# Kernel tuning notes

Measured on AMD Instinct MI355X. Metric: run time of the kernel, lower is better.

## Reference

```python
import jax, jax.numpy as jnp
import numpy as np

EPS = 1e-5
DN = ('NCHW', 'OIHW', 'NCHW')


def conv3x3(x, w, b):
    y = jax.lax.conv_general_dilated(x, w, window_strides=(1, 1), padding='SAME',
                                     dimension_numbers=DN)
    return y + b[None, :, None, None]


def bn_relu(x, g, be, m, v):
    # inference-mode BatchNorm2d followed by ReLU, folded into one FMA
    inv = g / jnp.sqrt(v + EPS)
    return jax.nn.relu(x * inv[None, :, None, None] + (be - m * inv)[None, :, None, None])


def haar_idwt2(cA, cH, cV, cD):
    # pywt.idwt2(coeffs, 'db1'): cH = detail along rows (axis -2), cV = detail along cols (axis -1)
    # Exact Haar synthesis -> 2x2 pixel blocks (pixel-shuffle style, no CPU round-trip)
    p00 = (cA + cH + cV + cD) * 0.5  # (2i,   2j)
    p01 = (cA + cH - cV - cD) * 0.5  # (2i,   2j+1)
    p10 = (cA - cH + cV - cD) * 0.5  # (2i+1, 2j)
    p11 = (cA - cH - cV + cD) * 0.5  # (2i+1, 2j+1)
    B, C, H, W = cA.shape
    even = jnp.stack([p00, p01], axis=-1).reshape(B, C, H, 2 * W)
    odd = jnp.stack([p10, p11], axis=-1).reshape(B, C, H, 2 * W)
    return jnp.stack([even, odd], axis=-2).reshape(B, C, 2 * H, 2 * W)


def setup_inputs() -> dict:
    key = jax.random.key(0)
    ks = jax.random.split(key, 24)
    B, IN_C, OUT_C, H, W = 16, 128, 64, 64, 64
    d = {}
    d['x'] = jax.random.normal(ks[0], (B, IN_C, H, W), jnp.float32)
    d['s'] = jax.random.normal(ks[1], (B, OUT_C, 2 * H, 2 * W), jnp.float32)
    # input_convdwt: Conv(in_c -> 4*in_c) + BN
    d['w1'] = jax.random.normal(ks[2], (4 * IN_C, IN_C, 3, 3), jnp.float32) * 0.05
    d['b1'] = jax.random.normal(ks[3], (4 * IN_C,), jnp.float32) * 0.05
    d['g1'] = jax.random.uniform(ks[4], (4 * IN_C,), jnp.float32, 0.5, 1.5)
    d['be1'] = jax.random.normal(ks[5], (4 * IN_C,), jnp.float32) * 0.05
    d['m1'] = jax.random.normal(ks[6], (4 * IN_C,), jnp.float32) * 0.05
    d['v1'] = jax.random.uniform(ks[7], (4 * IN_C,), jnp.float32, 0.5, 1.5)
    # s_con: Conv(in_c -> out_c) + BN
    d['ws'] = jax.random.normal(ks[8], (OUT_C, IN_C, 3, 3), jnp.float32) * 0.05
    d['bs'] = jax.random.normal(ks[9], (OUT_C,), jnp.float32) * 0.05
    d['gs'] = jax.random.uniform(ks[10], (OUT_C,), jnp.float32, 0.5, 1.5)
    d['bes'] = jax.random.normal(ks[11], (OUT_C,), jnp.float32) * 0.05
    d['ms'] = jax.random.normal(ks[12], (OUT_C,), jnp.float32) * 0.05
    d['vs'] = jax.random.uniform(ks[13], (OUT_C,), jnp.float32, 0.5, 1.5)
    # conv: Conv(in_c -> out_c) + BN (applied to concat(s, s_out))
    d['w2'] = jax.random.normal(ks[14], (OUT_C, IN_C, 3, 3), jnp.float32) * 0.05
    d['b2'] = jax.random.normal(ks[15], (OUT_C,), jnp.float32) * 0.05
    d['g2'] = jax.random.uniform(ks[16], (OUT_C,), jnp.float32, 0.5, 1.5)
    d['be2'] = jax.random.normal(ks[17], (OUT_C,), jnp.float32) * 0.05
    d['m2'] = jax.random.normal(ks[18], (OUT_C,), jnp.float32) * 0.05
    d['v2'] = jax.random.uniform(ks[19], (OUT_C,), jnp.float32, 0.5, 1.5)
    return d


def reference(x, s, w1, b1, g1, be1, m1, v1,
              ws, bs, gs, bes, ms, vs,
              w2, b2, g2, be2, m2, v2):
    # input_convdwt: conv -> BN -> ReLU, channels in_c -> 4*in_c
    h = bn_relu(conv3x3(x, w1, b1), g1, be1, m1, v1)
    c = h.shape[1]
    q = c // 4
    cA, cH, cV, cD = h[:, :q], h[:, q:2 * q], h[:, 2 * q:3 * q], h[:, 3 * q:]
    idwt_out = haar_idwt2(cA, cH, cV, cD)  # (B, in_c, 2H, 2W)
    # skip-connection branch (s is not None)
    s_out = bn_relu(conv3x3(idwt_out, ws, bs), gs, bes, ms, vs)  # (B, out_c, 2H, 2W)
    concat = jnp.concatenate([s, s_out], axis=1)                  # (B, in_c, 2H, 2W)
    decoder_output = bn_relu(conv3x3(concat, w2, b2), g2, be2, m2, v2)
    return decoder_output
```

## Files before the change

kernel.cpp:

```cpp
#include <hip/hip_runtime.h>
#include <hip/hip_bf16.h>

typedef __attribute__((ext_vector_type(8))) short short8;
typedef __attribute__((ext_vector_type(4))) float f32x4;
typedef unsigned short u16;

#define EPSV 1e-5f

__device__ __forceinline__ u16 f2bf(float f) {
    __hip_bfloat16 h = __float2bfloat16(f);
    return *reinterpret_cast<u16*>(&h);
}

#define GLOAD_LDS16(g, l)                                                      \
    __builtin_amdgcn_global_load_lds(                                          \
        (const __attribute__((address_space(1))) void*)(g),                    \
        (__attribute__((address_space(3))) void*)(l), 16, 0, 0)

__global__ void cvt_kernel(const float* __restrict__ src, u16* __restrict__ dst,
                           int C, int H, int W, int units) {
    int u = blockIdx.x * 256 + threadIdx.x;
    if (u >= units) return;
    int kb = u & 3;
    int p  = u >> 2;
    int x  = p % W;  p /= W;
    int y  = p % H;  p /= H;
    int n  = p & 15;
    int cc = p >> 4;
    short8 v;
#pragma unroll
    for (int j = 0; j < 8; ++j)
        v[j] = (short)f2bf(src[(((size_t)n * C + cc * 32 + kb * 8 + j) * H + y) * W + x]);
    *(short8*)(dst + ((((size_t)cc * 16 + n) * H + y) * W + x) * 32 + kb * 8) = v;
}

__global__ void repack_w1_kernel(const float* __restrict__ w1, u16* __restrict__ wf) {
    int u = blockIdx.x * 256 + threadIdx.x;
    if (u >= 4 * 8 * 9 * 4 * 64) return;
    int l = u & 63;
    int r = u >> 6;
    int ciC = r & 3;  r >>= 2;
    int t   = r % 9;  r /= 9;
    int bt  = r & 7;
    int cc  = r >> 3;
    int co  = (bt >> 1) * 128 + cc * 32 + (bt & 1) * 16 + (l & 15);
    int ci0 = ciC * 32 + (l >> 4) * 8;
    short8 v;
#pragma unroll
    for (int e = 0; e < 8; ++e)
        v[e] = (short)f2bf(w1[((size_t)co * 128 + ci0 + e) * 9 + t]);
    *(short8*)(wf + (size_t)u * 8) = v;
}

__global__ void repack_wg_kernel(const float* __restrict__ w, u16* __restrict__ wf) {
    int u = blockIdx.x * 256 + threadIdx.x;
    if (u >= 4 * 9 * 4 * 64) return;
    int l = u & 63;
    int r = u >> 6;
    int ciC = r & 3;  r >>= 2;
    int t   = r % 9;
    int bt  = r / 9;
    int co  = bt * 16 + (l & 15);
    int ci0 = ciC * 32 + (l >> 4) * 8;
    short8 v;
#pragma unroll
    for (int e = 0; e < 8; ++e)
        v[e] = (short)f2bf(w[((size_t)co * 128 + ci0 + e) * 9 + t]);
    *(short8*)(wf + (size_t)u * 8) = v;
}

__global__ __launch_bounds__(256, 2)
void conv1_mfma_kernel(const u16* __restrict__ inb, const u16* __restrict__ wf,
                       const float* __restrict__ bb, const float* __restrict__ gg,
                       const float* __restrict__ bee, const float* __restrict__ mm,
                       const float* __restrict__ vv, u16* __restrict__ ob) {
    const int tile = blockIdx.x;
    const int cc   = blockIdx.y;
    const int n    = blockIdx.z;
    const int x0   = (tile & 3) * 16;
    const int y0   = (tile >> 2) * 8;
    const int tid  = threadIdx.x;
    const int lane = tid & 63;
    const int wid  = tid >> 6;
    const int wm   = wid >> 1;
    const int wc   = wid & 1;
    const int kb   = lane >> 4;
    const int xl   = lane & 15;

    __shared__ float4 lds4[720];
    __shared__ float4 wlds[2][1536];
    const short8* ldsr  = (const short8*)lds4;
    const short8* wldsr = (const short8*)wlds;

    f32x4 acc[4][4];
#pragma unroll
    for (int j = 0; j < 4; ++j)
#pragma unroll
        for (int q = 0; q < 4; ++q) acc[j][q] = (f32x4){0.f, 0.f, 0.f, 0.f};

    float4 sreg[3];
    auto load_stage = [&](int ciC) {
#pragma unroll
        for (int p = 0; p < 3; ++p) {
            int e = p * 256 + tid;
            float4 v = make_float4(0.f, 0.f, 0.f, 0.f);
            if (e < 720) {
                int pix = e >> 2, ke = e & 3;
                int yy = pix / 18;
                int xx = pix - yy * 18;
                int gy = y0 - 1 + yy, gx = x0 - 1 + xx;
                if ((unsigned)gy < 64u && (unsigned)gx < 64u)
                    v = *(const float4*)(inb + ((((size_t)ciC * 16 + n) * 64 + gy) * 64 + gx) * 32 + ke * 8);
            }
            sreg[p] = v;
        }
    };
    auto write_stage = [&]() {
#pragma unroll
        for (int p = 0; p < 3; ++p) {
            int e = p * 256 + tid;
            if (e < 720) lds4[e ^ ((e >> 2) & 7)] = sreg[p];
        }
    };
    auto stage_w = [&](int ciC, int dx, int buf) {
#pragma unroll
        for (int i = 0; i < 6; ++i) {
            int seg = wid * 6 + i;
            int bt  = seg / 3;
            int dy  = seg - bt * 3;
            int t   = dy * 3 + dx;
            const u16* gp = wf + (size_t)((cc * 8 + bt) * 9 + t) * 2048 + ciC * 512 + lane * 8;
            GLOAD_LDS16(gp, &wlds[buf][seg * 64]);
        }
    };

    load_stage(0);
    stage_w(0, 0, 0);
    for (int ciC = 0; ciC < 4; ++ciC) {
        write_stage();
        asm volatile("s_waitcnt lgkmcnt(0)" ::: "memory");
        __builtin_amdgcn_s_barrier();
        __builtin_amdgcn_sched_barrier(0);
        if (ciC < 3) load_stage(ciC + 1);
#pragma unroll
        for (int dx = 0; dx < 3; ++dx) {
            const int cur = (ciC + dx) & 1;
            if (dx == 0) {
                if (ciC < 3) asm volatile("s_waitcnt vmcnt(3)" ::: "memory");
                else         asm volatile("s_waitcnt vmcnt(0)" ::: "memory");
            } else {
                asm volatile("s_waitcnt vmcnt(0)" ::: "memory");
            }
            __builtin_amdgcn_sched_barrier(0);
            __builtin_amdgcn_s_barrier();
            __builtin_amdgcn_sched_barrier(0);
            if (dx < 2)        stage_w(ciC, dx + 1, cur ^ 1);
            else if (ciC < 3)  stage_w(ciC + 1, 0, cur ^ 1);

            short8 a[6];
#pragma unroll
            for (int r = 0; r < 6; ++r) {
                int pix = (wm * 4 + r) * 18 + xl + dx;
                int e = pix * 4 + kb;
                a[r] = ldsr[e ^ ((e >> 2) & 7)];
            }
#pragma unroll
            for (int dy = 0; dy < 3; ++dy) {
                short8 b[4];
#pragma unroll
                for (int q = 0; q < 4; ++q) {
                    int bt = q * 2 + wc;
                    b[q] = wldsr[cur * 1536 + (bt * 3 + dy) * 64 + lane];
                }
#pragma unroll
                for (int j = 0; j < 4; ++j)
#pragma unroll
                    for (int q = 0; q < 4; ++q)
                        acc[j][q] = __builtin_amdgcn_mfma_f32_16x16x32_bf16(a[j + dy], b[q], acc[j][q], 0, 0, 0);
            }
        }
        __builtin_amdgcn_s_barrier();
    }

    float invq[4], shq[4];
#pragma unroll
    for (int q = 0; q < 4; ++q) {
        int co  = q * 128 + cc * 32 + wc * 16 + xl;
        float inv = gg[co] / sqrtf(vv[co] + EPSV);
        invq[q] = inv;
        shq[q]  = bb[co] * inv + bee[co] - mm[co] * inv;
    }
    const int c32 = wc * 16 + xl;
#pragma unroll
    for (int j = 0; j < 4; ++j) {
        int y = y0 + wm * 4 + j;
#pragma unroll
        for (int i = 0; i < 4; ++i) {
            float A_ = fmaxf(acc[j][0][i] * invq[0] + shq[0], 0.f);
            float H_ = fmaxf(acc[j][1][i] * invq[1] + shq[1], 0.f);
            float V_ = fmaxf(acc[j][2][i] * invq[2] + shq[2], 0.f);
            float D_ = fmaxf(acc[j][3][i] * invq[3] + shq[3], 0.f);
            float p00 = (A_ + H_ + V_ + D_) * 0.5f;
            float p01 = (A_ + H_ - V_ - D_) * 0.5f;
            float p10 = (A_ - H_ + V_ - D_) * 0.5f;
            float p11 = (A_ - H_ - V_ + D_) * 0.5f;
            int oy = 2 * y, ox = 2 * (x0 + kb * 4 + i);
            size_t base = ((((size_t)cc * 16 + n) * 128 + oy) * 128 + ox) * 32 + c32;
            ob[base]            = f2bf(p00);
            ob[base + 32]       = f2bf(p01);
            ob[base + 128 * 32] = f2bf(p10);
            ob[base + 128 * 32 + 32] = f2bf(p11);
        }
    }
}

template <bool FP32OUT, bool SFUSE>
__global__ __launch_bounds__(256, 2)
void convg_mfma_kernel(const u16* __restrict__ inb, const float* __restrict__ sfp,
                       const u16* __restrict__ wf,
                       const float* __restrict__ bb, const float* __restrict__ gg,
                       const float* __restrict__ bee, const float* __restrict__ mm,
                       const float* __restrict__ vv, u16* __restrict__ ob,
                       float* __restrict__ of) {
    const int tile = blockIdx.x;
    const int n    = blockIdx.y;
    const int x0   = (tile & 7) * 16;
    const int y0   = (tile >> 3) * 8;
    const int tid  = threadIdx.x;
    const int lane = tid & 63;
    const int wid  = tid >> 6;
    const int wm   = wid >> 1;
    const int wc   = wid & 1;
    const int kb   = lane >> 4;
    const int xl   = lane & 15;

    __shared__ float4 lds4[720];
    __shared__ float4 wlds[2][768];
    const short8* ldsr  = (const short8*)lds4;
    const short8* wldsr = (const short8*)wlds;

    f32x4 acc[4][2];
#pragma unroll
    for (int j = 0; j < 4; ++j)
#pragma unroll
        for (int cb = 0; cb < 2; ++cb) acc[j][cb] = (f32x4){0.f, 0.f, 0.f, 0.f};

    float4 sreg[3];
    auto load_stage = [&](int ciC) {
#pragma unroll
        for (int p = 0; p < 3; ++p) {
            int e = p * 256 + tid;
            float4 v = make_float4(0.f, 0.f, 0.f, 0.f);
            if (e < 720) {
                int pix = e >> 2, ke = e & 3;
                int yy = pix / 18;
                int xx = pix - yy * 18;
                int gy = y0 - 1 + yy, gx = x0 - 1 + xx;
                bool ib = (unsigned)gy < 128u && (unsigned)gx < 128u;
                if (SFUSE && ciC < 2) {
                    if (ib) {
                        const float* sp = sfp + (((size_t)n * 64 + ciC * 32 + ke * 8) * 128 + gy) * 128 + gx;
                        short8 sv;
#pragma unroll
                        for (int j = 0; j < 8; ++j)
                            sv[j] = (short)f2bf(sp[(size_t)j * 16384]);
                        v = *(float4*)&sv;
                    }
                } else if (ib) {
                    v = *(const float4*)(inb + ((((size_t)ciC * 16 + n) * 128 + gy) * 128 + gx) * 32 + ke * 8);
                }
            }
            sreg[p] = v;
        }
    };
    auto write_stage = [&]() {
#pragma unroll
        for (int p = 0; p < 3; ++p) {
            int e = p * 256 + tid;
            if (e < 720) lds4[e ^ ((e >> 2) & 7)] = sreg[p];
        }
    };
    auto stage_w = [&](int ciC, int dx, int buf) {
#pragma unroll
        for (int i = 0; i < 3; ++i) {
            int seg = wid * 3 + i;
            int bt  = seg / 3;
            int dy  = seg - bt * 3;
            int t   = dy * 3 + dx;
            const u16* gp = wf + (size_t)(((bt * 9 + t) * 4 + ciC) * 64 + lane) * 8;
            GLOAD_LDS16(gp, &wlds[buf][seg * 64]);
        }
    };

    load_stage(0);
    stage_w(0, 0, 0);
    for (int ciC = 0; ciC < 4; ++ciC) {
        write_stage();
        asm volatile("s_waitcnt lgkmcnt(0)" ::: "memory");
        __builtin_amdgcn_s_barrier();
        __builtin_amdgcn_sched_barrier(0);
#pragma unroll
        for (int dx = 0; dx < 3; ++dx) {
            const int cur = (ciC + dx) & 1;
            asm volatile("s_waitcnt vmcnt(0)" ::: "memory");
            __builtin_amdgcn_sched_barrier(0);
            __builtin_amdgcn_s_barrier();
            __builtin_amdgcn_sched_barrier(0);
            if (dx < 2)        stage_w(ciC, dx + 1, cur ^ 1);
            else if (ciC < 3)  stage_w(ciC + 1, 0, cur ^ 1);
            if (dx == 0 && ciC < 3) load_stage(ciC + 1);

            short8 a[6];
#pragma unroll
            for (int r = 0; r < 6; ++r) {
                int pix = (wm * 4 + r) * 18 + xl + dx;
                int e = pix * 4 + kb;
                a[r] = ldsr[e ^ ((e >> 2) & 7)];
            }
#pragma unroll
            for (int dy = 0; dy < 3; ++dy) {
                short8 b[2];
#pragma unroll
                for (int cb = 0; cb < 2; ++cb) {
                    int bt = wc * 2 + cb;
                    b[cb] = wldsr[cur * 768 + (bt * 3 + dy) * 64 + lane];
                }
#pragma unroll
                for (int j = 0; j < 4; ++j)
#pragma unroll
                    for (int cb = 0; cb < 2; ++cb)
                        acc[j][cb] = __builtin_amdgcn_mfma_f32_16x16x32_bf16(a[j + dy], b[cb], acc[j][cb], 0, 0, 0);
            }
        }
        __builtin_amdgcn_s_barrier();
    }

#pragma unroll
    for (int cb = 0; cb < 2; ++cb) {
        int co = (wc * 2 + cb) * 16 + xl;
        float inv = gg[co] / sqrtf(vv[co] + EPSV);
        float sh  = bb[co] * inv + bee[co] - mm[co] * inv;
#pragma unroll
        for (int j = 0; j < 4; ++j) {
            int y = y0 + wm * 4 + j;
            if (FP32OUT) {
                float4 v4;
                v4.x = fmaxf(acc[j][cb][0] * inv + sh, 0.f);
                v4.y = fmaxf(acc[j][cb][1] * inv + sh, 0.f);
                v4.z = fmaxf(acc[j][cb][2] * inv + sh, 0.f);
                v4.w = fmaxf(acc[j][cb][3] * inv + sh, 0.f);
                *(float4*)&of[(((size_t)n * 64 + co) * 128 + y) * 128 + x0 + kb * 4] = v4;
            } else {
#pragma unroll
                for (int i = 0; i < 4; ++i) {
                    float val = fmaxf(acc[j][cb][i] * inv + sh, 0.f);
                    int xg = x0 + kb * 4 + i;
                    ob[((((size_t)(co >> 5) * 16 + n) * 128 + y) * 128 + xg) * 32 + (co & 31)] = f2bf(val);
                }
            }
        }
    }
}

extern "C" void kernel_launch(void* const* d_in, const int* in_sizes, int n_in,
                              void* d_out, int out_size, void* d_ws, size_t ws_size,
                              hipStream_t stream) {
    const float* x   = (const float*)d_in[0];
    const float* s   = (const float*)d_in[1];
    const float* w1  = (const float*)d_in[2];
    const float* b1  = (const float*)d_in[3];
    const float* g1  = (const float*)d_in[4];
    const float* be1 = (const float*)d_in[5];
    const float* m1  = (const float*)d_in[6];
    const float* v1  = (const float*)d_in[7];
    const float* wsw = (const float*)d_in[8];
    const float* bs  = (const float*)d_in[9];
    const float* gs  = (const float*)d_in[10];
    const float* bes = (const float*)d_in[11];
    const float* ms  = (const float*)d_in[12];
    const float* vs  = (const float*)d_in[13];
    const float* w2  = (const float*)d_in[14];
    const float* b2  = (const float*)d_in[15];
    const float* g2  = (const float*)d_in[16];
    const float* be2 = (const float*)d_in[17];
    const float* m2  = (const float*)d_in[18];
    const float* v2  = (const float*)d_in[19];
    float* out = (float*)d_out;

    char* wsp = (char*)d_ws;
    u16* xb   = (u16*)(wsp);
    u16* idwt = (u16*)(wsp + 16777216);
    u16* cat  = (u16*)(wsp + 16777216 + 67108864);
    u16* wf1  = (u16*)(wsp + 16777216 + 67108864 + 67108864);
    u16* wfS  = (u16*)(wsp + 16777216 + 67108864 + 67108864 + 1179648);
    u16* wf2  = (u16*)(wsp + 16777216 + 67108864 + 67108864 + 1179648 + 147456);

    cvt_kernel<<<dim3(4096), dim3(256), 0, stream>>>(x, xb, 128, 64, 64, 1048576);
    repack_w1_kernel<<<dim3(288), dim3(256), 0, stream>>>(w1, wf1);
    repack_wg_kernel<<<dim3(36), dim3(256), 0, stream>>>(wsw, wfS);
    repack_wg_kernel<<<dim3(36), dim3(256), 0, stream>>>(w2, wf2);

    conv1_mfma_kernel<<<dim3(32, 4, 16), dim3(256), 0, stream>>>(
        xb, wf1, b1, g1, be1, m1, v1, idwt);

    convg_mfma_kernel<false, false><<<dim3(128, 16), dim3(256), 0, stream>>>(
        idwt, nullptr, wfS, bs, gs, bes, ms, vs,
        cat + (size_t)2 * 16 * 128 * 128 * 32, nullptr);

    convg_mfma_kernel<true, true><<<dim3(128, 16), dim3(256), 0, stream>>>(
        cat, s, wf2, b2, g2, be2, m2, v2, nullptr, out);
}
```

Measured before the change: 213.8 us.

## Pre-convert skip tensor to bf16 and relax weight-load wait in grouped conv

Drops the fused on-the-fly fp32-to-bf16 gather of the skip tensor s inside the final conv, which did eight strided scalar loads per 16-byte element. A separate cvt kernel now writes s into the concat buffer in the blocked bf16 layout. The conv's stage loads become uniform vector loads. The dx==1 step now waits with vmcnt(3) instead of vmcnt(0), so the next input stage's loads can stay in flight while the weight loads complete. The cost is an extra kernel launch plus a write and read of the converted s through memory, and the partial wait depends on the exact order in which loads are issued.

```diff
diff --git a/kernel.cpp b/kernel.cpp
--- a/kernel.cpp
+++ b/kernel.cpp
@@ -214,10 +214,9 @@
     }
 }
 
-template <bool FP32OUT, bool SFUSE>
+template <bool FP32OUT>
 __global__ __launch_bounds__(256, 2)
-void convg_mfma_kernel(const u16* __restrict__ inb, const float* __restrict__ sfp,
-                       const u16* __restrict__ wf,
+void convg_mfma_kernel(const u16* __restrict__ inb, const u16* __restrict__ wf,
                        const float* __restrict__ bb, const float* __restrict__ gg,
                        const float* __restrict__ bee, const float* __restrict__ mm,
                        const float* __restrict__ vv, u16* __restrict__ ob,
@@ -256,19 +255,8 @@
                 int yy = pix / 18;
                 int xx = pix - yy * 18;
                 int gy = y0 - 1 + yy, gx = x0 - 1 + xx;
-                bool ib = (unsigned)gy < 128u && (unsigned)gx < 128u;
-                if (SFUSE && ciC < 2) {
-                    if (ib) {
-                        const float* sp = sfp + (((size_t)n * 64 + ciC * 32 + ke * 8) * 128 + gy) * 128 + gx;
-                        short8 sv;
-#pragma unroll
-                        for (int j = 0; j < 8; ++j)
-                            sv[j] = (short)f2bf(sp[(size_t)j * 16384]);
-                        v = *(float4*)&sv;
-                    }
-                } else if (ib) {
+                if ((unsigned)gy < 128u && (unsigned)gx < 128u)
                     v = *(const float4*)(inb + ((((size_t)ciC * 16 + n) * 128 + gy) * 128 + gx) * 32 + ke * 8);
-                }
             }
             sreg[p] = v;
         }
@@ -302,7 +290,8 @@
 #pragma unroll
         for (int dx = 0; dx < 3; ++dx) {
             const int cur = (ciC + dx) & 1;
-            asm volatile("s_waitcnt vmcnt(0)" ::: "memory");
+            if (dx == 1 && ciC < 3) asm volatile("s_waitcnt vmcnt(3)" ::: "memory");
+            else                    asm volatile("s_waitcnt vmcnt(0)" ::: "memory");
             __builtin_amdgcn_sched_barrier(0);
             __builtin_amdgcn_s_barrier();
             __builtin_amdgcn_sched_barrier(0);
@@ -396,6 +385,7 @@
     u16* wf2  = (u16*)(wsp + 16777216 + 67108864 + 67108864 + 1179648 + 147456);
 
     cvt_kernel<<<dim3(4096), dim3(256), 0, stream>>>(x, xb, 128, 64, 64, 1048576);
+    cvt_kernel<<<dim3(8192), dim3(256), 0, stream>>>(s, cat, 64, 128, 128, 2097152);
     repack_w1_kernel<<<dim3(288), dim3(256), 0, stream>>>(w1, wf1);
     repack_wg_kernel<<<dim3(36), dim3(256), 0, stream>>>(wsw, wfS);
     repack_wg_kernel<<<dim3(36), dim3(256), 0, stream>>>(w2, wf2);
@@ -403,10 +393,10 @@
     conv1_mfma_kernel<<<dim3(32, 4, 16), dim3(256), 0, stream>>>(
         xb, wf1, b1, g1, be1, m1, v1, idwt);
 
-    convg_mfma_kernel<false, false><<<dim3(128, 16), dim3(256), 0, stream>>>(
-        idwt, nullptr, wfS, bs, gs, bes, ms, vs,
+    convg_mfma_kernel<false><<<dim3(128, 16), dim3(256), 0, stream>>>(
+        idwt, wfS, bs, gs, bes, ms, vs,
         cat + (size_t)2 * 16 * 128 * 128 * 32, nullptr);
 
-    convg_mfma_kernel<true, true><<<dim3(128, 16), dim3(256), 0, stream>>>(
-        cat, s, wf2, b2, g2, be2, m2, v2, nullptr, out);
-}
+    convg_mfma_kernel<true><<<dim3(128, 16), dim3(256), 0, stream>>>(
+        cat, wf2, b2, g2, be2, m2, v2, nullptr, out);
+}
```

After: 215.6 us. Within noise of the previous version (+0.8%).
